# Kernel tuning notes

Hardware: AMD Instinct MI355X
Metric: run time of the kernel (lower is better)

## Reference

```python
import jax, jax.numpy as jnp
import numpy as np

B, S, D, H, KD, HID = 8, 1024, 512, 8, 64, 32


def setup_inputs() -> dict:
    key = jax.random.key(0)
    ks = jax.random.split(key, 13)
    s = 0.05
    return {
        "src": jax.random.normal(ks[0], (B, S, D), jnp.float32),
        "Wq": jax.random.normal(ks[1], (H, KD, D), jnp.float32) * s,
        "Wk": jax.random.normal(ks[2], (H, KD, D), jnp.float32) * s,
        "Wv": jax.random.normal(ks[3], (H, KD, D), jnp.float32) * s,
        "c_raw": jnp.ones((H,), jnp.float32),              # nn.Parameter(1.0) per head
        "L": jnp.full((H,), 2.0, jnp.float32),             # nn.Parameter(2.0) per head
        "w1": jax.random.normal(ks[4], (H, HID), jnp.float32) * s,   # Linear(1,HID) weight
        "b1": jax.random.normal(ks[5], (H, HID), jnp.float32) * s,
        "W2": jax.random.normal(ks[6], (H, HID, HID), jnp.float32) * s,  # [out,in]
        "b2": jax.random.normal(ks[7], (H, HID), jnp.float32) * s,
        "w3": jax.random.normal(ks[8], (H, HID), jnp.float32) * s,   # Linear(HID,1) weight
        "b3": jax.random.normal(ks[9], (H,), jnp.float32) * s,
        "Wo": jax.random.normal(ks[10], (D, D), jnp.float32) * s,
    }


def _gelu(x):
    return jax.nn.gelu(x, approximate=False)  # torch nn.GELU default (erf)


def reference(src, Wq, Wk, Wv, c_raw, L, w1, b1, W2, b2, w3, b3, Wo):
    Bc, Sc, Dc = src.shape
    Hh, Kd = Wq.shape[0], Wq.shape[1]
    # ---- FIRE bias: raw[i,j] = log1p(c*(i-j)) / log1p(c*max(L, i+1)) for j<i else 0
    ii = jnp.arange(Sc, dtype=jnp.float32)[:, None]   # [S,1]
    jj = jnp.arange(Sc, dtype=jnp.float32)[None, :]   # [1,S]
    d = ii - jj                                       # [S,S]
    c = jax.nn.softplus(c_raw)[:, None, None]         # [H,1,1]
    num = jnp.log1p(c * jnp.where(d > 0, d, 1.0)[None])          # safe for d<=0
    den = jnp.log1p(c * jnp.maximum(L[:, None, None], ii[None] + 1.0))
    raw = jnp.where(d[None] > 0, num / den, 0.0)      # [H,S,S]
    # ---- f_theta MLP applied elementwise (Linear(1,h)->GELU->Linear(h,h)->GELU->Linear(h,1))
    h1 = _gelu(raw[..., None] * w1[:, None, None, :] + b1[:, None, None, :])   # [H,S,S,HID]
    h2 = _gelu(jnp.einsum('hijk,hlk->hijl', h1, W2) + b2[:, None, None, :])    # [H,S,S,HID]
    bias = jnp.einsum('hijk,hk->hij', h2, w3) + b3[:, None, None]              # [H,S,S]
    # ---- causal mask (strict upper triangle -> -inf)
    causal = jnp.arange(Sc)[None, :] > jnp.arange(Sc)[:, None]
    bias = jnp.where(causal[None], -jnp.inf, bias)
    # ---- attention per head
    q = jnp.einsum('bsd,hkd->bhsk', src, Wq)
    k = jnp.einsum('bsd,hkd->bhsk', src, Wk)
    v = jnp.einsum('bsd,hkd->bhsk', src, Wv)
    logits = jnp.einsum('bhik,bhjk->bhij', q, k) / jnp.sqrt(jnp.float32(Kd)) + bias[None]
    attn = jax.nn.softmax(logits, axis=-1)
    o = jnp.einsum('bhij,bhjk->bhik', attn, v)        # [B,H,S,KD]
    o = jnp.transpose(o, (0, 2, 1, 3)).reshape(Bc, Sc, Hh * Kd)  # concat heads
    return o @ Wo.T
```

## Files before the change

kernel.cpp:

```cpp
#include <hip/hip_runtime.h>
#include <math.h>

#define S_LEN 1024
#define NHEAD 8
#define BATCH 8
#define KDIM  64
#define HID   32
#define NT    2048
#define TRI(q) ((q) * ((q) + 1) / 2)
#define PERM(m) (((m) & 0x20) | (((m) & 0x0C) << 1) | (((m) & 0x10) >> 2) | ((m) & 3))
#define SWZ(row) (((((row) >> 3) & 1) << 2) | ((row) & 3))

typedef __attribute__((ext_vector_type(8))) short bf16x8;
typedef __attribute__((ext_vector_type(4))) float f32x4;
typedef unsigned short ushort_t;

__device__ inline ushort_t f2bf(float f) {
  union { float f; unsigned u; } v; v.f = f;
  unsigned u = v.u;
  return (ushort_t)((u + 0x7FFFu + ((u >> 16) & 1u)) >> 16);
}
__device__ inline float bf2f(ushort_t u) {
  union { unsigned x; float f; } v; v.x = ((unsigned)u) << 16; return v.f;
}

__device__ inline void gl_lds16(const ushort_t* g, ushort_t* l) {
  __builtin_amdgcn_global_load_lds(
      (const __attribute__((address_space(1))) unsigned int*)g,
      (__attribute__((address_space(3))) unsigned int*)l, 16, 0, 0);
}

__global__ __launch_bounds__(256) void prep(
    const float* __restrict__ s, const float* __restrict__ wq,
    const float* __restrict__ wk, const float* __restrict__ wv,
    const float* __restrict__ wo,
    ushort_t* __restrict__ sb, ushort_t* __restrict__ wqb,
    ushort_t* __restrict__ wkb, ushort_t* __restrict__ wvb,
    ushort_t* __restrict__ wob,
    const float* __restrict__ c_raw, const float* __restrict__ Lp,
    const float* __restrict__ w1, const float* __restrict__ b1,
    const float* __restrict__ W2, const float* __restrict__ b2,
    const float* __restrict__ w3, const float* __restrict__ b3,
    float* __restrict__ num_g, float* __restrict__ rden_g,
    float* __restrict__ gtab_g) {
  __shared__ float h1s[8][33];
  const int bx = blockIdx.x;
  const int tid = threadIdx.x;
  if (bx < 5120) {
    const float* src; ushort_t* dst; int base; float scale = 1.0f;
    if (bx < 4096)      { src = s;  dst = sb;  base = bx; }
    else if (bx < 4352) { src = wq; dst = wqb; base = bx - 4096; scale = 0.125f; }
    else if (bx < 4608) { src = wk; dst = wkb; base = bx - 4352; }
    else if (bx < 4864) { src = wv; dst = wvb; base = bx - 4608; }
    else                { src = wo; dst = wob; base = bx - 4864; }
    const int i = (base * 256 + tid) * 4;
    float4 v = *(const float4*)&src[i];
    ushort4 o;
    o.x = f2bf(v.x * scale); o.y = f2bf(v.y * scale);
    o.z = f2bf(v.z * scale); o.w = f2bf(v.w * scale);
    *(ushort4*)&dst[i] = o;
  } else {
    const int idx = bx - 5120;
    const int h = idx / 257;
    const int xb = idx % 257;
    const float cr = c_raw[h];
    const float c = (cr > 20.f) ? cr : log1pf(expf(cr));
    const int gid = xb * 256 + tid;
    if (gid < S_LEN) {
      num_g[h * S_LEN + gid] = log1pf(c * (float)gid);
      rden_g[h * S_LEN + gid] = 1.0f / log1pf(c * fmaxf(Lp[h], (float)(gid + 1)));
    }
    const int pl = tid >> 5;
    const int j = tid & 31;
    const int pt = xb * 8 + pl;
    const float x = (float)pt * (1.0f / NT);
    float v = x * w1[h * HID + j] + b1[h * HID + j];
    h1s[pl][j] = 0.5f * v * (1.0f + erff(v * 0.70710678118f));
    __syncthreads();
    float sm = b2[h * HID + j];
    const float* w2r = W2 + ((size_t)(h * HID + j)) * HID;
    #pragma unroll
    for (int k = 0; k < HID; ++k) sm += w2r[k] * h1s[pl][k];
    float g = 0.5f * sm * (1.0f + erff(sm * 0.70710678118f));
    float y = w3[h * HID + j] * g;
    #pragma unroll
    for (int off = 1; off < 32; off <<= 1) y += __shfl_xor(y, off);
    if (j == 0 && pt <= NT) gtab_g[h * (NT + 1) + pt] = y + b3[h];
  }
}

__device__ __forceinline__ void gemm_tile(
    ushort_t* sAB, const ushort_t* __restrict__ A, const ushort_t* __restrict__ Wp,
    void* __restrict__ outp, int mode, int m0, int n0, int tid) {
  ushort_t* sA = sAB;
  ushort_t* sB = sAB + 4096;
  const int lane = tid & 63, w = tid >> 6, quad = lane >> 4, l16 = lane & 15;
  f32x4 acc[4];
  #pragma unroll
  for (int nb = 0; nb < 4; ++nb) acc[nb] = (f32x4)0.0f;

  const int r8 = lane >> 3;
  const int gc = (lane & 7) ^ r8;
  const int sw = l16 & 7;

  for (int kt = 0; kt < 512; kt += 64) {
    __syncthreads();
    #pragma unroll
    for (int j = 0; j < 2; ++j) {
      const int row = w * 16 + j * 8 + r8;
      gl_lds16(&A[(size_t)(m0 + row) * 512 + kt + gc * 8], &sA[(w * 16 + j * 8) * 64]);
      gl_lds16(&Wp[(size_t)(n0 + row) * 512 + kt + gc * 8], &sB[(w * 16 + j * 8) * 64]);
    }
    __syncthreads();
    #pragma unroll
    for (int ks = 0; ks < 2; ++ks) {
      const int off = ((ks * 4 + quad) ^ sw) * 8;
      bf16x8 af = *(bf16x8*)&sA[(w * 16 + l16) * 64 + off];
      #pragma unroll
      for (int nb = 0; nb < 4; ++nb) {
        bf16x8 bfr = *(bf16x8*)&sB[(nb * 16 + l16) * 64 + off];
        acc[nb] = __builtin_amdgcn_mfma_f32_16x16x32_bf16(af, bfr, acc[nb], 0, 0, 0);
      }
    }
  }

  if (mode == 2) {
    __syncthreads();
    #pragma unroll
    for (int nb = 0; nb < 4; ++nb)
      #pragma unroll
      for (int r = 0; r < 4; ++r) {
        int nl = nb * 16 + l16;
        int ml = w * 16 + quad * 4 + r;
        sAB[nl * 64 + (((ml >> 3) ^ (nl & 7)) * 8) + (ml & 7)] = f2bf(acc[nb][r]);
      }
    __syncthreads();
    const int nl = tid >> 2, seg = tid & 3;
    const int ng = n0 + nl, hh = ng >> 6, kd = ng & 63;
    const int bb = m0 >> 10, sbase = m0 & 1023;
    ushort_t* vout = (ushort_t*)outp + (((size_t)(bb * NHEAD + hh)) * KDIM + kd) * S_LEN;
    #pragma unroll
    for (int c2 = 0; c2 < 2; ++c2) {
      int mc = seg * 2 + c2;
      bf16x8 vr = *(bf16x8*)&sAB[nl * 64 + ((mc ^ (nl & 7)) * 8)];
      *(bf16x8*)&vout[sbase + mc * 8] = vr;
    }
    return;
  }
  #pragma unroll
  for (int nb = 0; nb < 4; ++nb) {
    #pragma unroll
    for (int r = 0; r < 4; ++r) {
      int m = m0 + w * 16 + quad * 4 + r;
      int n = n0 + nb * 16 + l16;
      float v = acc[nb][r];
      if (mode == 1) {
        int bb = m >> 10, ss = m & 1023, hh = n >> 6, kd = n & 63;
        ((ushort_t*)outp)[(((size_t)(bb * NHEAD + hh)) * S_LEN + ss) * KDIM + kd] = f2bf(v);
      } else {
        ((float*)outp)[(size_t)m * 512 + n] = v;
      }
    }
  }
}

__global__ __launch_bounds__(256) void gemm_bias(
    const ushort_t* __restrict__ A,
    const ushort_t* __restrict__ W0, const ushort_t* __restrict__ W1,
    const ushort_t* __restrict__ W2w,
    void* __restrict__ out0, void* __restrict__ out1, void* __restrict__ out2,
    int scatter, int nGemm,
    const float* __restrict__ num_g, const float* __restrict__ rden_g,
    const float* __restrict__ gtab_g, ushort_t* __restrict__ biaspre) {
  __shared__ __align__(16) ushort_t sAB[8192];
  const int tid = threadIdx.x;
  if ((int)blockIdx.x < nGemm) {
    int z, tile;
    if (scatter) { z = blockIdx.x % 3; tile = blockIdx.x / 3; }
    else         { z = 0;              tile = blockIdx.x; }
    const int m0 = (tile & 127) * 64;
    const int n0 = (tile >> 7) * 64;
    const ushort_t* Wp = (z == 0) ? W0 : (z == 1) ? W1 : W2w;
    void* outp = (z == 0) ? out0 : (z == 1) ? out1 : out2;
    const int mode = scatter ? ((z == 2) ? 2 : 1) : 0;
    gemm_tile(sAB, A, Wp, outp, mode, m0, n0, tid);
  } else {
    const int idx = blockIdx.x - nGemm;
    const int h = idx / 68;
    const int pair = idx % 68;
    float* gtab_s = (float*)sAB;
    float* num_s = gtab_s + 2052;
    float* rden_s = num_s + 1024;
    for (int i = tid; i <= NT; i += 256) gtab_s[i] = gtab_g[h * (NT + 1) + i];
    for (int i = tid; i < S_LEN; i += 256) num_s[i] = num_g[h * S_LEN + i];
    const int sub = tid >> 7, tid2 = tid & 127;
    const int tileIdx = pair * 2 + sub;
    int qt = 0;
    while (TRI(qt + 1) <= tileIdx) ++qt;
    const int t = tileIdx - TRI(qt);
    if (tid2 < 64) rden_s[sub * 64 + tid2] = rden_g[h * S_LEN + qt * 64 + tid2];
    __syncthreads();
    const int w = tid2 >> 6, lane = tid2 & 63, quad = lane >> 4, l16 = lane & 15;
    ushort_t vals[32];
    #pragma unroll
    for (int qg = 0; qg < 2; ++qg) {
      const int iloc = w * 32 + qg * 16 + l16;
      const int i = qt * 64 + iloc;
      const float rden = rden_s[sub * 64 + iloc];
      #pragma unroll
      for (int nb = 0; nb < 4; ++nb)
        #pragma unroll
        for (int r = 0; r < 4; ++r) {
          const int m = nb * 16 + quad * 4 + r;
          const int j = t * 64 + PERM(m);
          ushort_t out;
          if (j > i) {
            out = 0xFF80;
          } else {
            const int d = i - j;
            float x = num_s[d] * rden;
            float tf = x * (float)NT;
            int it = (int)tf; it = it < (NT - 1) ? it : (NT - 1);
            float fr = tf - (float)it;
            float ga = gtab_s[it];
            out = f2bf(ga + (gtab_s[it + 1] - ga) * fr);
          }
          vals[qg * 16 + nb * 4 + r] = out;
        }
    }
    ushort_t* dst = &biaspre[((size_t)(h * 136 + tileIdx) * 128 + tid2) * 32];
    uint4 u[2];
    #pragma unroll
    for (int half = 0; half < 2; ++half) {
      #pragma unroll
      for (int v = 0; v < 8; ++v) ((ushort_t*)&u[0])[v] = vals[half * 16 + v];
      #pragma unroll
      for (int v = 0; v < 8; ++v) ((ushort_t*)&u[1])[v] = vals[half * 16 + 8 + v];
      *(uint4*)(dst + half * 16) = u[0];
      *(uint4*)(dst + half * 16 + 8) = u[1];
    }
  }
}

__global__ __launch_bounds__(128) void fire_attn_mfma(
    const ushort_t* __restrict__ Qg, const ushort_t* __restrict__ Kg,
    const ushort_t* __restrict__ Vtg, const ushort_t* __restrict__ biaspre,
    ushort_t* __restrict__ Ob) {
  __shared__ __align__(16) ushort_t Ks[64 * 64];
  __shared__ __align__(16) ushort_t Vt[64 * 64];
  const int tid = threadIdx.x;
  const int lane = tid & 63, w = tid >> 6, quad = lane >> 4, l16 = lane & 15;
  const int g = blockIdx.x >> 6;
  const int qt = (g < 8) ? (15 - g) : (g - 8);
  const int bh = blockIdx.x & 63, h = bh & 7, b = bh >> 3;

  bf16x8 q[2][2];
  {
    const size_t qb = (size_t)bh * S_LEN + qt * 64 + w * 32;
    #pragma unroll
    for (int qg = 0; qg < 2; ++qg)
      #pragma unroll
      for (int ks = 0; ks < 2; ++ks)
        q[qg][ks] = *(const bf16x8*)&Qg[(qb + qg * 16 + l16) * KDIM + ks * 32 + quad * 8];
  }

  const size_t kb = (size_t)bh * S_LEN * KDIM;
  const ushort_t* bptr = &biaspre[((size_t)(h * 136 + TRI(qt)) * 128 + tid) * 32];
  const int srow8 = lane >> 3;
  const int sc = lane & 7;

  f32x4 o[2][4];
  float ll[2] = {0.f, 0.f};
  #pragma unroll
  for (int qg = 0; qg < 2; ++qg)
    #pragma unroll
    for (int nb = 0; nb < 4; ++nb) o[qg][nb] = (f32x4)0.0f;

  for (int t = 0; t <= qt; ++t) {
    __syncthreads();
    #pragma unroll
    for (int j = 0; j < 4; ++j) {
      const int row = (w * 4 + j) * 8 + srow8;
      const int cc = sc ^ SWZ(row);
      gl_lds16(&Kg[kb + (size_t)(t * 64 + row) * 64 + cc * 8], &Ks[(w * 4 + j) * 512]);
      gl_lds16(&Vtg[kb + (size_t)row * 1024 + t * 64 + cc * 8], &Vt[(w * 4 + j) * 512]);
    }
    __syncthreads();

    uint4 bb0 = ((const uint4*)(bptr + (size_t)t * 4096))[0];
    uint4 bb1 = ((const uint4*)(bptr + (size_t)t * 4096))[1];
    uint4 bb2 = ((const uint4*)(bptr + (size_t)t * 4096))[2];
    uint4 bb3 = ((const uint4*)(bptr + (size_t)t * 4096))[3];

    f32x4 s[2][4];
    #pragma unroll
    for (int qg = 0; qg < 2; ++qg)
      #pragma unroll
      for (int nb = 0; nb < 4; ++nb) s[qg][nb] = (f32x4)0.0f;
    #pragma unroll
    for (int ks = 0; ks < 2; ++ks) {
      #pragma unroll
      for (int nb = 0; nb < 4; ++nb) {
        const int rk = PERM(nb * 16 + l16);
        bf16x8 ak = *(bf16x8*)&Ks[rk * 64 + (((ks * 4 + quad) ^ SWZ(rk)) * 8)];
        #pragma unroll
        for (int qg = 0; qg < 2; ++qg)
          s[qg][nb] = __builtin_amdgcn_mfma_f32_16x16x32_bf16(ak, q[qg][ks], s[qg][nb], 0, 0, 0);
      }
    }

    ushort_t eb[2][16];
    #pragma unroll
    for (int qg = 0; qg < 2; ++qg) {
      #pragma unroll
      for (int nb = 0; nb < 4; ++nb)
        #pragma unroll
        for (int r = 0; r < 4; ++r) {
          const int v = qg * 16 + nb * 4 + r;
          const uint4& bq = (v < 8) ? bb0 : (v < 16) ? bb1 : (v < 24) ? bb2 : bb3;
          ushort_t bu = ((const ushort_t*)&bq)[v & 7];
          float p = __expf(s[qg][nb][r] + bf2f(bu));
          ll[qg] += p;
          eb[qg][nb * 4 + r] = f2bf(p);
        }
    }

    #pragma unroll
    for (int ks = 0; ks < 2; ++ks) {
      bf16x8 pf[2];
      #pragma unroll
      for (int qg = 0; qg < 2; ++qg) {
        union { bf16x8 v; unsigned u[4]; } pkx;
        pkx.u[0] = (unsigned)eb[qg][(2 * ks) * 4 + 0] | ((unsigned)eb[qg][(2 * ks) * 4 + 1] << 16);
        pkx.u[1] = (unsigned)eb[qg][(2 * ks) * 4 + 2] | ((unsigned)eb[qg][(2 * ks) * 4 + 3] << 16);
        pkx.u[2] = (unsigned)eb[qg][(2 * ks + 1) * 4 + 0] | ((unsigned)eb[qg][(2 * ks + 1) * 4 + 1] << 16);
        pkx.u[3] = (unsigned)eb[qg][(2 * ks + 1) * 4 + 2] | ((unsigned)eb[qg][(2 * ks + 1) * 4 + 3] << 16);
        pf[qg] = pkx.v;
      }
      #pragma unroll
      for (int nb = 0; nb < 4; ++nb) {
        const int rv = nb * 16 + l16;
        bf16x8 av = *(bf16x8*)&Vt[rv * 64 + (((ks * 4 + quad) ^ SWZ(rv)) * 8)];
        #pragma unroll
        for (int qg = 0; qg < 2; ++qg)
          o[qg][nb] = __builtin_amdgcn_mfma_f32_16x16x32_bf16(av, pf[qg], o[qg][nb], 0, 0, 0);
      }
    }
  }

  #pragma unroll
  for (int qg = 0; qg < 2; ++qg) {
    float rs = ll[qg];
    rs += __shfl_xor(rs, 16);
    rs += __shfl_xor(rs, 32);
    const float rl = 1.0f / rs;
    const size_t ob = ((size_t)(b * S_LEN + qt * 64 + w * 32 + qg * 16 + l16)) * 512 + h * KDIM;
    #pragma unroll
    for (int nb = 0; nb < 4; ++nb) {
      ushort4 ov;
      ov.x = f2bf(o[qg][nb][0] * rl);
      ov.y = f2bf(o[qg][nb][1] * rl);
      ov.z = f2bf(o[qg][nb][2] * rl);
      ov.w = f2bf(o[qg][nb][3] * rl);
      *(ushort4*)&Ob[ob + nb * 16 + quad * 4] = ov;
    }
  }
}

extern "C" void kernel_launch(void* const* d_in, const int* in_sizes, int n_in,
                              void* d_out, int out_size, void* d_ws, size_t ws_size,
                              hipStream_t stream) {
  const float* src   = (const float*)d_in[0];
  const float* Wq    = (const float*)d_in[1];
  const float* Wk    = (const float*)d_in[2];
  const float* Wv    = (const float*)d_in[3];
  const float* c_raw = (const float*)d_in[4];
  const float* Lp    = (const float*)d_in[5];
  const float* w1    = (const float*)d_in[6];
  const float* b1    = (const float*)d_in[7];
  const float* W2    = (const float*)d_in[8];
  const float* b2    = (const float*)d_in[9];
  const float* w3    = (const float*)d_in[10];
  const float* b3    = (const float*)d_in[11];
  const float* Wo    = (const float*)d_in[12];
  float* outp = (float*)d_out;

  const size_t SRC_E = 4194304;
  const size_t W_E   = 262144;
  const size_t QKV_E = 4194304;
  ushort_t* srcb = (ushort_t*)d_ws;
  ushort_t* Wqb  = srcb + SRC_E;
  ushort_t* Wkb  = Wqb + W_E;
  ushort_t* Wvb  = Wkb + W_E;
  ushort_t* Wob  = Wvb + W_E;
  ushort_t* Qb   = Wob + W_E;
  ushort_t* Kb   = Qb + QKV_E;
  ushort_t* Vtb  = Kb + QKV_E;
  ushort_t* Obb  = Vtb + QKV_E;
  ushort_t* biaspre = Obb + QKV_E;
  float* numb  = (float*)(biaspre + (size_t)NHEAD * 136 * 128 * 32);
  float* rdenb = numb + NHEAD * S_LEN;
  float* gtabb = rdenb + NHEAD * S_LEN;

  hipLaunchKernelGGL(prep, dim3(7176), dim3(256), 0, stream,
                     src, Wq, Wk, Wv, Wo, srcb, Wqb, Wkb, Wvb, Wob,
                     c_raw, Lp, w1, b1, W2, b2, w3, b3, numb, rdenb, gtabb);
  hipLaunchKernelGGL(gemm_bias, dim3(3616), dim3(256), 0, stream,
                     srcb, Wqb, Wkb, Wvb, (void*)Qb, (void*)Kb, (void*)Vtb,
                     1, 3072, numb, rdenb, gtabb, biaspre);
  hipLaunchKernelGGL(fire_attn_mfma, dim3(1024), dim3(128), 0, stream,
                     Qb, Kb, Vtb, biaspre, Obb);
  hipLaunchKernelGGL(gemm_bias, dim3(1024), dim3(256), 0, stream,
                     Obb, Wob, Wob, Wob, (void*)outp, (void*)outp, (void*)outp,
                     0, 1024, numb, rdenb, gtabb, biaspre);
}
```

Measured before the change: 166.4 us.

## Load K/V fragments directly from global and keep full weight panel in LDS

The attention kernel drops its LDS staging of K and V tiles and their block barriers, and instead has each lane read its MFMA fragments straight from global memory (relying on L1/L2 caching). The projection GEMM now stages the whole 64x512 weight panel into LDS once, streams A fragments directly from global, and reorders block indices so the tiles sharing an A row-block are adjacent. This removes per-k-step barriers and LDS round trips. In exchange it issues more uncoalesced global loads and uses 64KB of LDS per GEMM block, which lowers occupancy.

```diff
diff --git a/kernel.cpp b/kernel.cpp
--- a/kernel.cpp
+++ b/kernel.cpp
@@ -9,7 +9,6 @@
 #define NT    2048
 #define TRI(q) ((q) * ((q) + 1) / 2)
 #define PERM(m) (((m) & 0x20) | (((m) & 0x0C) << 1) | (((m) & 0x10) >> 2) | ((m) & 3))
-#define SWZ(row) (((((row) >> 3) & 1) << 2) | ((row) & 3))
 
 typedef __attribute__((ext_vector_type(8))) short bf16x8;
 typedef __attribute__((ext_vector_type(4))) float f32x4;
@@ -90,37 +89,32 @@
 }
 
 __device__ __forceinline__ void gemm_tile(
-    ushort_t* sAB, const ushort_t* __restrict__ A, const ushort_t* __restrict__ Wp,
+    ushort_t* sB, const ushort_t* __restrict__ A, const ushort_t* __restrict__ Wp,
     void* __restrict__ outp, int mode, int m0, int n0, int tid) {
-  ushort_t* sA = sAB;
-  ushort_t* sB = sAB + 4096;
   const int lane = tid & 63, w = tid >> 6, quad = lane >> 4, l16 = lane & 15;
+
+  #pragma unroll
+  for (int i = 0; i < 16; ++i) {
+    const int r = w * 16 + i;
+    gl_lds16(&Wp[(size_t)(n0 + r) * 512 + ((lane ^ (r & 7)) * 8)], &sB[r * 512]);
+  }
+  __syncthreads();
+
   f32x4 acc[4];
   #pragma unroll
   for (int nb = 0; nb < 4; ++nb) acc[nb] = (f32x4)0.0f;
 
-  const int r8 = lane >> 3;
-  const int gc = (lane & 7) ^ r8;
+  const ushort_t* arow = &A[(size_t)(m0 + w * 16 + l16) * 512];
   const int sw = l16 & 7;
 
-  for (int kt = 0; kt < 512; kt += 64) {
-    __syncthreads();
-    #pragma unroll
-    for (int j = 0; j < 2; ++j) {
-      const int row = w * 16 + j * 8 + r8;
-      gl_lds16(&A[(size_t)(m0 + row) * 512 + kt + gc * 8], &sA[(w * 16 + j * 8) * 64]);
-      gl_lds16(&Wp[(size_t)(n0 + row) * 512 + kt + gc * 8], &sB[(w * 16 + j * 8) * 64]);
-    }
-    __syncthreads();
-    #pragma unroll
-    for (int ks = 0; ks < 2; ++ks) {
-      const int off = ((ks * 4 + quad) ^ sw) * 8;
-      bf16x8 af = *(bf16x8*)&sA[(w * 16 + l16) * 64 + off];
-      #pragma unroll
-      for (int nb = 0; nb < 4; ++nb) {
-        bf16x8 bfr = *(bf16x8*)&sB[(nb * 16 + l16) * 64 + off];
-        acc[nb] = __builtin_amdgcn_mfma_f32_16x16x32_bf16(af, bfr, acc[nb], 0, 0, 0);
-      }
+  #pragma unroll 4
+  for (int kt = 0; kt < 16; ++kt) {
+    bf16x8 af = *(const bf16x8*)&arow[kt * 32 + quad * 8];
+    #pragma unroll
+    for (int nb = 0; nb < 4; ++nb) {
+      const int row = nb * 16 + l16;
+      bf16x8 bfr = *(bf16x8*)&sB[row * 512 + (((kt * 4 + quad) ^ sw) * 8)];
+      acc[nb] = __builtin_amdgcn_mfma_f32_16x16x32_bf16(af, bfr, acc[nb], 0, 0, 0);
     }
   }
 
@@ -132,7 +126,7 @@
       for (int r = 0; r < 4; ++r) {
         int nl = nb * 16 + l16;
         int ml = w * 16 + quad * 4 + r;
-        sAB[nl * 64 + (((ml >> 3) ^ (nl & 7)) * 8) + (ml & 7)] = f2bf(acc[nb][r]);
+        sB[nl * 64 + (((ml >> 3) ^ (nl & 7)) * 8) + (ml & 7)] = f2bf(acc[nb][r]);
       }
     __syncthreads();
     const int nl = tid >> 2, seg = tid & 3;
@@ -142,7 +136,7 @@
     #pragma unroll
     for (int c2 = 0; c2 < 2; ++c2) {
       int mc = seg * 2 + c2;
-      bf16x8 vr = *(bf16x8*)&sAB[nl * 64 + ((mc ^ (nl & 7)) * 8)];
+      bf16x8 vr = *(bf16x8*)&sB[nl * 64 + ((mc ^ (nl & 7)) * 8)];
       *(bf16x8*)&vout[sbase + mc * 8] = vr;
     }
     return;
@@ -172,23 +166,29 @@
     int scatter, int nGemm,
     const float* __restrict__ num_g, const float* __restrict__ rden_g,
     const float* __restrict__ gtab_g, ushort_t* __restrict__ biaspre) {
-  __shared__ __align__(16) ushort_t sAB[8192];
+  __shared__ __align__(16) ushort_t sB[32768];
   const int tid = threadIdx.x;
   if ((int)blockIdx.x < nGemm) {
-    int z, tile;
-    if (scatter) { z = blockIdx.x % 3; tile = blockIdx.x / 3; }
-    else         { z = 0;              tile = blockIdx.x; }
-    const int m0 = (tile & 127) * 64;
-    const int n0 = (tile >> 7) * 64;
+    int z, m0, n0;
+    if (scatter) {
+      const int nz = blockIdx.x % 24;
+      m0 = (blockIdx.x / 24) * 64;
+      z = nz % 3;
+      n0 = (nz / 3) * 64;
+    } else {
+      m0 = (blockIdx.x >> 3) * 64;
+      n0 = (blockIdx.x & 7) * 64;
+      z = 0;
+    }
     const ushort_t* Wp = (z == 0) ? W0 : (z == 1) ? W1 : W2w;
     void* outp = (z == 0) ? out0 : (z == 1) ? out1 : out2;
     const int mode = scatter ? ((z == 2) ? 2 : 1) : 0;
-    gemm_tile(sAB, A, Wp, outp, mode, m0, n0, tid);
+    gemm_tile(sB, A, Wp, outp, mode, m0, n0, tid);
   } else {
     const int idx = blockIdx.x - nGemm;
     const int h = idx / 68;
     const int pair = idx % 68;
-    float* gtab_s = (float*)sAB;
+    float* gtab_s = (float*)sB;
     float* num_s = gtab_s + 2052;
     float* rden_s = num_s + 1024;
     for (int i = tid; i <= NT; i += 256) gtab_s[i] = gtab_g[h * (NT + 1) + i];
@@ -246,8 +246,6 @@
     const ushort_t* __restrict__ Qg, const ushort_t* __restrict__ Kg,
     const ushort_t* __restrict__ Vtg, const ushort_t* __restrict__ biaspre,
     ushort_t* __restrict__ Ob) {
-  __shared__ __align__(16) ushort_t Ks[64 * 64];
-  __shared__ __align__(16) ushort_t Vt[64 * 64];
   const int tid = threadIdx.x;
   const int lane = tid & 63, w = tid >> 6, quad = lane >> 4, l16 = lane & 15;
   const int g = blockIdx.x >> 6;
@@ -266,8 +264,13 @@
 
   const size_t kb = (size_t)bh * S_LEN * KDIM;
   const ushort_t* bptr = &biaspre[((size_t)(h * 136 + TRI(qt)) * 128 + tid) * 32];
-  const int srow8 = lane >> 3;
-  const int sc = lane & 7;
+  const ushort_t* kgrow[4];
+  const ushort_t* vgrow[4];
+  #pragma unroll
+  for (int nb = 0; nb < 4; ++nb) {
+    kgrow[nb] = &Kg[kb + (size_t)PERM(nb * 16 + l16) * 64 + quad * 8];
+    vgrow[nb] = &Vtg[kb + (size_t)(nb * 16 + l16) * 1024 + quad * 8];
+  }
 
   f32x4 o[2][4];
   float ll[2] = {0.f, 0.f};
@@ -277,16 +280,6 @@
     for (int nb = 0; nb < 4; ++nb) o[qg][nb] = (f32x4)0.0f;
 
   for (int t = 0; t <= qt; ++t) {
-    __syncthreads();
-    #pragma unroll
-    for (int j = 0; j < 4; ++j) {
-      const int row = (w * 4 + j) * 8 + srow8;
-      const int cc = sc ^ SWZ(row);
-      gl_lds16(&Kg[kb + (size_t)(t * 64 + row) * 64 + cc * 8], &Ks[(w * 4 + j) * 512]);
-      gl_lds16(&Vtg[kb + (size_t)row * 1024 + t * 64 + cc * 8], &Vt[(w * 4 + j) * 512]);
-    }
-    __syncthreads();
-
     uint4 bb0 = ((const uint4*)(bptr + (size_t)t * 4096))[0];
     uint4 bb1 = ((const uint4*)(bptr + (size_t)t * 4096))[1];
     uint4 bb2 = ((const uint4*)(bptr + (size_t)t * 4096))[2];
@@ -301,8 +294,7 @@
     for (int ks = 0; ks < 2; ++ks) {
       #pragma unroll
       for (int nb = 0; nb < 4; ++nb) {
-        const int rk = PERM(nb * 16 + l16);
-        bf16x8 ak = *(bf16x8*)&Ks[rk * 64 + (((ks * 4 + quad) ^ SWZ(rk)) * 8)];
+        bf16x8 ak = *(const bf16x8*)(kgrow[nb] + (size_t)t * 4096 + ks * 32);
         #pragma unroll
         for (int qg = 0; qg < 2; ++qg)
           s[qg][nb] = __builtin_amdgcn_mfma_f32_16x16x32_bf16(ak, q[qg][ks], s[qg][nb], 0, 0, 0);
@@ -339,8 +331,7 @@
       }
       #pragma unroll
       for (int nb = 0; nb < 4; ++nb) {
-        const int rv = nb * 16 + l16;
-        bf16x8 av = *(bf16x8*)&Vt[rv * 64 + (((ks * 4 + quad) ^ SWZ(rv)) * 8)];
+        bf16x8 av = *(const bf16x8*)(vgrow[nb] + (size_t)t * 64 + ks * 32);
         #pragma unroll
         for (int qg = 0; qg < 2; ++qg)
           o[qg][nb] = __builtin_amdgcn_mfma_f32_16x16x32_bf16(av, pf[qg], o[qg][nb], 0, 0, 0);
```

After: 216.2 us. 30.0% more time.
